# Optimization experiments

Hardware: AMD Instinct MI355X
Metric: run time of the kernel (lower is better)

The kernel has to match this reference:

```python
import jax, jax.numpy as jnp
import numpy as np

IGNORE = 255
THRESH = 0.7
MIN_KEPT = 100000
AUX_W = 1.0


def resize_bilinear_ac(x, oh, ow):
    # F.interpolate(..., mode='bilinear', align_corners=True); x: (b,c,h,w)
    b, c, h, w = x.shape
    ys = jnp.linspace(0.0, h - 1.0, oh)
    xs = jnp.linspace(0.0, w - 1.0, ow)
    y0 = jnp.floor(ys).astype(jnp.int32)
    x0 = jnp.floor(xs).astype(jnp.int32)
    y1 = jnp.minimum(y0 + 1, h - 1)
    x1 = jnp.minimum(x0 + 1, w - 1)
    wy = (ys - y0)[:, None]          # (oh,1) broadcasts over (b,c,oh,w)
    wx = xs - x0                     # (ow,)
    rows = x[:, :, y0, :] * (1.0 - wy) + x[:, :, y1, :] * wy   # (b,c,oh,w)
    return rows[:, :, :, x0] * (1.0 - wx) + rows[:, :, :, x1] * wx


def ohem_ce(pred, target):
    # pred: (b,c,h,w) logits, target: (b,h,w) int labels
    b, c, h, w = pred.shape
    n = b * h * w
    t = target.reshape(-1)
    valid = t != IGNORE
    t_cl = jnp.where(valid, t, 0)
    logits = pred.transpose(0, 2, 3, 1).reshape(n, c)
    logp = jax.nn.log_softmax(logits, axis=-1)
    pix = jnp.arange(n)
    logp_t = logp[pix, t_cl]
    # prob at target class; invalid pixels filled with 1 (as in masked_fill_)
    mask_prob = jnp.where(valid, jnp.exp(logp_t), 1.0)
    idx = min(n, MIN_KEPT) - 1
    thr = jnp.maximum(jnp.asarray(THRESH, pred.dtype), jnp.sort(mask_prob)[idx])
    kept = mask_prob <= thr
    final_valid = valid & kept
    nll = -logp_t
    denom = jnp.maximum(final_valid.sum(), 1).astype(pred.dtype)
    return jnp.sum(jnp.where(final_valid, nll, 0.0)) / denom


def boundary_bce(p, t):
    # p: (n,1,h,w) probs, t: (n,1,h,w) binary targets; per-sample pos/neg weights
    pos = jnp.sum(t == 1.0, axis=(1, 2, 3), keepdims=True).astype(p.dtype)
    neg = jnp.sum(t == 0.0, axis=(1, 2, 3), keepdims=True).astype(p.dtype)
    valid = pos + neg
    wgt = jnp.where(t == 1.0, neg / valid, jnp.where(t == 0.0, pos / valid, 0.0))
    logp = jnp.clip(jnp.log(p), -100.0)          # torch BCELoss clamps log at -100
    log1mp = jnp.clip(jnp.log(1.0 - p), -100.0)
    bce = -(t * logp + (1.0 - t) * log1mp)
    return jnp.mean(wgt * bce)


def setup_inputs() -> dict:
    key = jax.random.key(0)
    k1, k2, k3, k4, k5 = jax.random.split(key, 5)
    main_pred = jax.random.normal(k1, (4, 19, 64, 128), dtype=jnp.float32)
    coarse_pred = jax.random.normal(k2, (4, 19, 64, 128), dtype=jnp.float32)
    boundary_pred = jax.random.uniform(k3, (4, 1, 64, 128), dtype=jnp.float32)
    seg_gt = jax.random.randint(k4, (4, 512, 1024), 0, 19, dtype=jnp.int32)
    boundary_gt = jax.random.randint(k5, (4, 1, 512, 1024), 0, 2).astype(jnp.float32)
    return {"main_pred": main_pred, "coarse_pred": coarse_pred,
            "boundary_pred": boundary_pred, "seg_gt": seg_gt,
            "boundary_gt": boundary_gt}


def reference(main_pred, coarse_pred, boundary_pred, seg_gt, boundary_gt):
    h, w = seg_gt.shape[1], seg_gt.shape[2]
    main_up = resize_bilinear_ac(main_pred, h, w)
    loss = ohem_ce(main_up, seg_gt)
    coarse_up = resize_bilinear_ac(coarse_pred, h, w)
    loss = loss + AUX_W * ohem_ce(coarse_up, seg_gt)
    bound_up = resize_bilinear_ac(boundary_pred, h, w)
    loss = loss + boundary_bce(bound_up, boundary_gt)
    return loss
```

## Files before the change

kernel.cpp:

```cpp
#include <hip/hip_runtime.h>

#define NPX    2097152
#define NPX4   (NPX/4)
#define CH_STR 8192
#define IMG_STR 155648

#define OFF_CTL   (2ull*NPX*4)
#define CTL_HIST    0
#define CTL_CNT1    0
#define CTL_CNT2    2048
#define CTL_BAR     24576
#define CTL_FLAG    24579
#define CTL_PREFIX  24580
#define CTL_KREM    24582
#define CTL_THR     24584
#define CTL_PPSUM   24586
#define CTL_PPCNT   28682
#define CTL_OPSUM   32778
#define CTL_OPCNT   33290
#define CTL_BPS     33802
#define CTL_BPC     34826

#define MAGIC_FAST 0x3A9C67E5u
#define GRID_P1    1536u

__device__ __forceinline__ void st_dev_f(float* p, float v) {
    __hip_atomic_store(p, v, __ATOMIC_RELAXED, __HIP_MEMORY_SCOPE_AGENT);
}
__device__ __forceinline__ void st_dev_u(unsigned* p, unsigned v) {
    __hip_atomic_store(p, v, __ATOMIC_RELAXED, __HIP_MEMORY_SCOPE_AGENT);
}
__device__ __forceinline__ float ld_dev_f(const float* p) {
    return __hip_atomic_load((float*)p, __ATOMIC_RELAXED, __HIP_MEMORY_SCOPE_AGENT);
}
__device__ __forceinline__ unsigned ld_dev_u(const unsigned* p) {
    return __hip_atomic_load((unsigned*)p, __ATOMIC_RELAXED, __HIP_MEMORY_SCOPE_AGENT);
}

__global__ __launch_bounds__(256, 5) void fused_pass1(
    const float* __restrict__ mp, const float* __restrict__ cp,
    const float* __restrict__ bp, const int* __restrict__ seg,
    const float* __restrict__ bg,
    float* __restrict__ probA, float* __restrict__ ppsum, unsigned* __restrict__ ppcnt,
    float* __restrict__ bps, unsigned* __restrict__ bpc,
    unsigned* __restrict__ cnt1, unsigned* __restrict__ cnt2,
    unsigned* __restrict__ flag,
    float* __restrict__ out)
{
    __shared__ float2 erow[19 * 128];
    __shared__ float rf[4]; __shared__ unsigned ru[4];
    __shared__ float rf2[4]; __shared__ unsigned ru2[4];
    __shared__ unsigned amLast;
    __shared__ float Pb[4], Nb[4]; __shared__ unsigned PCb[4], NCb[4];
    int bk = blockIdx.x;
    int tid = threadIdx.x;

    if (bk < 1024) {
        int v = ((bk & 7) << 7) | (bk >> 3);
        int head = v >> 9;
        int b    = (v >> 7) & 3;
        int k    = v & 127;
        const float* pred = head ? cp : mp;

        int y0g = min((int)((float)(4 * k) * (63.0f / 511.0f)), 63);
        int row0 = y0g, row1 = min(y0g + 1, 63), row2 = min(y0g + 2, 63);

        float4 rv[3][3];
#pragma unroll
        for (int r = 0; r < 3; ++r) {
            int ry = (r == 0) ? row0 : ((r == 1) ? row1 : row2);
            const float* rp = pred + (size_t)b * IMG_STR + ry * 128;
#pragma unroll
            for (int sr = 0; sr < 3; ++sr) {
                int s = tid + (sr << 8);
                if (s < 608) {
                    int c = s >> 5, x4 = (s & 31) << 2;
                    rv[r][sr] = *(const float4*)(rp + c * CH_STR + x4);
                } else {
                    rv[r][sr] = make_float4(0.f, 0.f, 0.f, 0.f);
                }
            }
        }

        int xb = tid << 2;
        float fx0 = (float)xb * (127.0f / 1023.0f);
        int X = min((int)fx0, 126);
        float wA[4], wB[4], wC[4];
#pragma unroll
        for (int dx = 0; dx < 4; ++dx) {
            float fx = (float)(xb + dx) * (127.0f / 1023.0f);
            int x0 = min((int)fx, 127);
            float wx = fx - (float)x0;
            bool sm = (x0 == X);
            wA[dx] = sm ? (1.0f - wx) : 0.0f;
            wB[dx] = sm ? wx : (1.0f - wx);
            wC[dx] = sm ? 0.0f : wx;
        }

#pragma unroll 1
        for (int d = 0; d < 4; ++d) {
            int y = (k << 2) + d;
            int task = (b << 9) + y;
            float fy = (float)y * (63.0f / 511.0f);
            int y0 = min((int)fy, 63);
            float wy = fy - (float)y0;
            int j = y0 - y0g;

            int P = task * 1024 + xb;
            int4 t4 = *(const int4*)(seg + P);
            int t[4] = {t4.x, t4.y, t4.z, t4.w};

#pragma unroll
            for (int sr = 0; sr < 3; ++sr) {
                int s = tid + (sr << 8);
                float4 cu = (j == 0) ? rv[0][sr] : rv[1][sr];
                float4 nx = (j == 0) ? rv[1][sr] : rv[2][sr];
                float e0 = fmaf(wy, nx.x - cu.x, cu.x);
                float e1 = fmaf(wy, nx.y - cu.y, cu.y);
                float e2 = fmaf(wy, nx.z - cu.z, cu.z);
                float e3 = fmaf(wy, nx.w - cu.w, cu.w);
                float en = __shfl_down(e0, 1, 64);
                if (s < 608) {
                    int c = s >> 5, x4 = (s & 31) << 2;
                    float last = ((s & 31) == 31) ? e3 : en;
                    float4 w0 = make_float4(e0, e1, e1, e2);
                    float4 w1 = make_float4(e2, e3, e3, last);
                    *(float4*)(&erow[c * 128 + x4])     = w0;
                    *(float4*)(&erow[c * 128 + x4 + 2]) = w1;
                }
            }
            __syncthreads();

            float acc[4] = {0.f, 0.f, 0.f, 0.f};
            for (int c = 0; c < 19; ++c) {
                float2 eA = erow[c * 128 + X];
                float2 eB = erow[c * 128 + X + 1];
#pragma unroll
                for (int dx = 0; dx < 4; ++dx) {
                    float l = fmaf(eA.x, wA[dx], fmaf(eA.y, wB[dx], eB.y * wC[dx]));
                    acc[dx] += __expf(l);
                }
            }

            float fs = 0.f; unsigned ic = 0;
            float pr[4];
#pragma unroll
            for (int dx = 0; dx < 4; ++dx) {
                bool valid = (t[dx] != 255);
                int tc = valid ? t[dx] : 0;
                float2 eA = erow[tc * 128 + X];
                float2 eB = erow[tc * 128 + X + 1];
                float lt = fmaf(eA.x, wA[dx], fmaf(eA.y, wB[dx], eB.y * wC[dx]));
                float ls = __logf(acc[dx]);
                float n  = ls - lt;
                float p  = fminf(__expf(-n), 1.0f);
                pr[dx] = valid ? p : 1.0f;
                if (valid && p <= 0.7f) { fs += n; ic++; }
            }
            *(float4*)(probA + (size_t)head * NPX + P) = make_float4(pr[0], pr[1], pr[2], pr[3]);

            for (int o = 32; o; o >>= 1) {
                fs += __shfl_down(fs, o, 64);
                ic += (unsigned)__shfl_down((int)ic, o, 64);
            }
            int wave = tid >> 6, lane = tid & 63;
            if (lane == 0) { rf[wave] = fs; ru[wave] = ic; }
            __syncthreads();
            if (tid == 0) {
                st_dev_f(&ppsum[head * 2048 + task], rf[0] + rf[1] + rf[2] + rf[3]);
                st_dev_u(&ppcnt[head * 2048 + task], ru[0] + ru[1] + ru[2] + ru[3]);
            }
        }
    } else {
        int bb = bk - 1024;
        int b  = bb >> 7;
        int blk = bb & 127;
        float psum = 0.f, nsum = 0.f; unsigned pc = 0, nc = 0;

        for (int g = blk * 256 + tid; g < 131072; g += 128 * 256) {
            int P = g << 2;
            int y = P >> 10, xb = P & 1023;

            float fy = (float)y * (63.0f / 511.0f);
            int y0 = min((int)fy, 63);
            int y1 = min(y0 + 1, 63);
            float wy = fy - (float)y0;

            const float* r0 = bp + b * 8192 + y0 * 128;
            const float* r1 = bp + b * 8192 + y1 * 128;
            float fx0 = (float)xb * (127.0f / 1023.0f);
            int X  = min((int)fx0, 126);
            int X2 = min(X + 2, 127);
            float c0 = r0[X], c1 = r0[X + 1], c2 = r0[X2];
            float d0 = r1[X], d1 = r1[X + 1], d2 = r1[X2];
            float e0 = fmaf(wy, d0 - c0, c0);
            float e1 = fmaf(wy, d1 - c1, c1);
            float e2 = fmaf(wy, d2 - c2, c2);

            float4 t4 = *(const float4*)(bg + (size_t)b * 524288 + P);
            float tv[4] = {t4.x, t4.y, t4.z, t4.w};

#pragma unroll
            for (int dx = 0; dx < 4; ++dx) {
                float fx = (float)(xb + dx) * (127.0f / 1023.0f);
                int x0 = min((int)fx, 127);
                int x1 = min(x0 + 1, 127);
                float wx = fx - (float)x0;
                float a0 = (x0 == X)     ? e0 : e1;
                float a1 = (x1 == X + 1) ? e1 : e2;
                float p  = fmaf(wx, a1 - a0, a0);
                bool isp = (tv[dx] == 1.0f);
                bool isn = (tv[dx] == 0.0f);
                float q = isp ? p : 1.0f - p;
                float l = fmaxf(__logf(q), -100.0f);
                if (isp) { pc++; psum -= l; }
                if (isn) { nc++; nsum -= l; }
            }
        }
        for (int o = 32; o; o >>= 1) {
            psum += __shfl_down(psum, o, 64);
            nsum += __shfl_down(nsum, o, 64);
            pc   += (unsigned)__shfl_down((int)pc, o, 64);
            nc   += (unsigned)__shfl_down((int)nc, o, 64);
        }
        int wave = tid >> 6, lane = tid & 63;
        if (lane == 0) { rf[wave] = psum; rf2[wave] = nsum; ru[wave] = pc; ru2[wave] = nc; }
        __syncthreads();
        if (tid == 0) {
            st_dev_f(&bps[2 * bb],     rf[0] + rf[1] + rf[2] + rf[3]);
            st_dev_f(&bps[2 * bb + 1], rf2[0] + rf2[1] + rf2[2] + rf2[3]);
            st_dev_u(&bpc[2 * bb],     ru[0] + ru[1] + ru[2] + ru[3]);
            st_dev_u(&bpc[2 * bb + 1], ru2[0] + ru2[1] + ru2[2] + ru2[3]);
        }
    }

    __syncthreads();
    if (tid == 0) {
        asm volatile("s_waitcnt vmcnt(0)" ::: "memory");
        unsigned last = 0u;
        unsigned o1 = __hip_atomic_fetch_add(&cnt1[(bk & 63) << 5], 1u,
                                             __ATOMIC_RELAXED, __HIP_MEMORY_SCOPE_AGENT);
        if (o1 == 23u) {
            unsigned o2 = __hip_atomic_fetch_add(cnt2, 1u,
                                                 __ATOMIC_RELAXED, __HIP_MEMORY_SCOPE_AGENT);
            last = (o2 == 63u) ? 1u : 0u;
        }
        amLast = last;
    }
    __syncthreads();
    if (!amLast) return;

    float s0 = 0.f, s1 = 0.f; unsigned c0 = 0u, c1 = 0u;
    for (int i = tid; i < 2048; i += 256) {
        s0 += ld_dev_f(&ppsum[i]);        c0 += ld_dev_u(&ppcnt[i]);
        s1 += ld_dev_f(&ppsum[2048 + i]); c1 += ld_dev_u(&ppcnt[2048 + i]);
    }
    for (int o = 32; o; o >>= 1) {
        s0 += __shfl_down(s0, o, 64); s1 += __shfl_down(s1, o, 64);
        c0 += (unsigned)__shfl_down((int)c0, o, 64);
        c1 += (unsigned)__shfl_down((int)c1, o, 64);
    }
    int wv = tid >> 6, ln = tid & 63;
    if (ln == 0) { rf[wv] = s0; rf2[wv] = s1; ru[wv] = c0; ru2[wv] = c1; }
    __syncthreads();
    float S0 = rf[0] + rf[1] + rf[2] + rf[3];
    float S1 = rf2[0] + rf2[1] + rf2[2] + rf2[3];
    unsigned C0 = ru[0] + ru[1] + ru[2] + ru[3];
    unsigned C1 = ru2[0] + ru2[1] + ru2[2] + ru2[3];
    bool fast = (C0 >= 100000u) && (C1 >= 100000u);

    if (fast) {
        float*    lf = (float*)erow;
        unsigned* lu = (unsigned*)erow + 256;
        for (int b = 0; b < 4; ++b) {
            float ps = 0.f, ns = 0.f; unsigned p_c = 0, n_c = 0;
            if (tid < 128) {
                int jj = b * 128 + tid;
                ps  = ld_dev_f(&bps[2 * jj]); ns  = ld_dev_f(&bps[2 * jj + 1]);
                p_c = ld_dev_u(&bpc[2 * jj]); n_c = ld_dev_u(&bpc[2 * jj + 1]);
            }
            lf[tid] = ps; lu[tid] = p_c; __syncthreads();
            for (int o = 128; o; o >>= 1) {
                if (tid < o) { lf[tid] += lf[tid + o]; lu[tid] += lu[tid + o]; }
                __syncthreads();
            }
            if (tid == 0) { Pb[b] = lf[0]; PCb[b] = lu[0]; }
            __syncthreads();
            lf[tid] = ns; lu[tid] = n_c; __syncthreads();
            for (int o = 128; o; o >>= 1) {
                if (tid < o) { lf[tid] += lf[tid + o]; lu[tid] += lu[tid + o]; }
                __syncthreads();
            }
            if (tid == 0) { Nb[b] = lf[0]; NCb[b] = lu[0]; }
            __syncthreads();
        }
        if (tid == 0) {
            float bt = 0.f;
            for (int b = 0; b < 4; ++b) {
                float pos = (float)PCb[b], neg = (float)NCb[b];
                float val = fmaxf(pos + neg, 1.f);
                bt += (neg / val) * Pb[b] + (pos / val) * Nb[b];
            }
            float hls = S0 / fmaxf((float)C0, 1.f) + S1 / fmaxf((float)C1, 1.f);
            out[0] = hls + bt / 2097152.0f;
            st_dev_u(flag, MAGIC_FAST);
        }
    }
}

__device__ __forceinline__ void gbar(unsigned* bar, int tid) {
    __syncthreads();
    if (tid == 0) {
        unsigned g = __hip_atomic_load(&bar[1], __ATOMIC_RELAXED, __HIP_MEMORY_SCOPE_AGENT);
        unsigned t = __hip_atomic_fetch_add(&bar[0], 1u, __ATOMIC_ACQ_REL, __HIP_MEMORY_SCOPE_AGENT);
        if (t == 255u) {
            __hip_atomic_store(&bar[0], 0u, __ATOMIC_RELAXED, __HIP_MEMORY_SCOPE_AGENT);
            __hip_atomic_store(&bar[1], g + 1u, __ATOMIC_RELEASE, __HIP_MEMORY_SCOPE_AGENT);
        } else {
            while (__hip_atomic_load(&bar[1], __ATOMIC_ACQUIRE, __HIP_MEMORY_SCOPE_AGENT) == g)
                __builtin_amdgcn_s_sleep(8);
        }
    }
    __syncthreads();
}

__device__ void combine_out(int tid, float headLossSum,
                            const float* __restrict__ bps, const unsigned* __restrict__ bpc,
                            float* __restrict__ out)
{
    __shared__ float lf[256]; __shared__ unsigned lu[256];
    __shared__ float Pb[4], Nb[4]; __shared__ unsigned PCb[4], NCb[4];
    for (int b = 0; b < 4; ++b) {
        float ps = 0.f, ns = 0.f; unsigned p_c = 0, n_c = 0;
        if (tid < 128) {
            int j = b * 128 + tid;
            ps = bps[2 * j]; ns = bps[2 * j + 1];
            p_c = bpc[2 * j]; n_c = bpc[2 * j + 1];
        }
        lf[tid] = ps; lu[tid] = p_c; __syncthreads();
        for (int o = 128; o; o >>= 1) {
            if (tid < o) { lf[tid] += lf[tid + o]; lu[tid] += lu[tid + o]; }
            __syncthreads();
        }
        if (tid == 0) { Pb[b] = lf[0]; PCb[b] = lu[0]; }
        __syncthreads();
        lf[tid] = ns; lu[tid] = n_c; __syncthreads();
        for (int o = 128; o; o >>= 1) {
            if (tid < o) { lf[tid] += lf[tid + o]; lu[tid] += lu[tid + o]; }
            __syncthreads();
        }
        if (tid == 0) { Nb[b] = lf[0]; NCb[b] = lu[0]; }
        __syncthreads();
    }
    if (tid == 0) {
        float bt = 0.f;
        for (int b = 0; b < 4; ++b) {
            float pos = (float)PCb[b], neg = (float)NCb[b];
            float val = fmaxf(pos + neg, 1.f);
            bt += (neg / val) * Pb[b] + (pos / val) * Nb[b];
        }
        out[0] = headLossSum + bt / 2097152.0f;
    }
}

__global__ __launch_bounds__(256) void finish_all(
    const float* __restrict__ probA, const int* __restrict__ seg,
    const float* __restrict__ ppsum, const unsigned* __restrict__ ppcnt,
    const float* __restrict__ bps, const unsigned* __restrict__ bpc,
    unsigned* __restrict__ hist, unsigned* __restrict__ bar,
    unsigned* __restrict__ prefix, unsigned* __restrict__ krem,
    float* __restrict__ thr,
    float* __restrict__ opsum, unsigned* __restrict__ opcnt,
    unsigned* __restrict__ flag,
    float* __restrict__ out)
{
    if (*flag == MAGIC_FAST)
        return;

    int tid = threadIdx.x, blk = blockIdx.x;
    int wave = tid >> 6, lane = tid & 63;

    float s0 = 0.f, s1 = 0.f; unsigned c0 = 0u, c1 = 0u;
    for (int i = tid; i < 2048; i += 256) {
        s0 += ppsum[i];        c0 += ppcnt[i];
        s1 += ppsum[2048 + i]; c1 += ppcnt[2048 + i];
    }
    for (int o = 32; o; o >>= 1) {
        s0 += __shfl_down(s0, o, 64); s1 += __shfl_down(s1, o, 64);
        c0 += (unsigned)__shfl_down((int)c0, o, 64);
        c1 += (unsigned)__shfl_down((int)c1, o, 64);
    }
    __shared__ float ws0[4], ws1[4]; __shared__ unsigned wc0[4], wc1[4];
    if (lane == 0) { ws0[wave] = s0; ws1[wave] = s1; wc0[wave] = c0; wc1[wave] = c1; }
    __syncthreads();
    float S0 = ws0[0] + ws0[1] + ws0[2] + ws0[3];
    float S1 = ws1[0] + ws1[1] + ws1[2] + ws1[3];
    unsigned C0 = wc0[0] + wc0[1] + wc0[2] + wc0[3];
    unsigned C1 = wc1[0] + wc1[1] + wc1[2] + wc1[3];
    bool done0 = C0 >= 100000u, done1 = C1 >= 100000u;

    if (done0 && done1) {
        if (blk == 0)
            combine_out(tid, S0 / fmaxf((float)C0, 1.f) + S1 / fmaxf((float)C1, 1.f),
                        bps, bpc, out);
        return;
    }

    __shared__ unsigned hsh[4096];
    __shared__ unsigned cpre[257];
    unsigned doneMask = (done0 ? 1u : 0u) | (done1 ? 2u : 0u);

    for (int i = blk * 256 + tid; i < 24576; i += 65536) hist[i] = 0u;
    gbar(bar, tid);

    for (int lvl = 0; lvl < 3; ++lvl) {
        unsigned* hl = hist + lvl * 8192;
        for (int h = 0; h < 2; ++h) {
            if (doneMask & (1u << h)) continue;
            unsigned pre = (lvl == 0) ? 0u : prefix[h];
            for (int i = tid; i < 4096; i += 256) hsh[i] = 0u;
            __syncthreads();
            const float4* prob = (const float4*)(probA + (size_t)h * NPX);
            for (int i = blk * 256 + tid; i < NPX4; i += 65536) {
                float4 p = prob[i];
                unsigned u[4] = {__float_as_uint(p.x), __float_as_uint(p.y),
                                 __float_as_uint(p.z), __float_as_uint(p.w)};
#pragma unroll
                for (int kk = 0; kk < 4; ++kk) {
                    unsigned bv = u[kk];
                    if (lvl == 0)      atomicAdd(&hsh[bv >> 18], 1u);
                    else if (lvl == 1) { if ((bv >> 18) == pre) atomicAdd(&hsh[(bv >> 6) & 0xFFFu], 1u); }
                    else               { if ((bv >> 6) == pre) atomicAdd(&hsh[bv & 63u], 1u); }
                }
            }
            __syncthreads();
            for (int i = tid; i < 4096; i += 256) {
                unsigned v = hsh[i];
                if (v) atomicAdd(&hl[h * 4096 + i], v);
            }
            __syncthreads();
        }
        gbar(bar, tid);
        if (blk == 0) {
            int bins = (lvl == 2) ? 64 : 4096;
            for (int h = 0; h < 2; ++h) {
                if (doneMask & (1u << h)) continue;
                const unsigned* hh = hl + h * 4096;
                int per = (bins + 255) >> 8;
                int base = tid * per;
                unsigned ssum = 0;
                for (int i = 0; i < per; ++i) { int idx = base + i; if (idx < bins) ssum += hh[idx]; }
                cpre[tid] = ssum; __syncthreads();
                if (tid == 0) {
                    unsigned acc = 0;
                    for (int i = 0; i < 256; ++i) { unsigned v = cpre[i]; cpre[i] = acc; acc += v; }
                    cpre[256] = acc;
                }
                __syncthreads();
                unsigned K = (lvl == 0) ? 100000u : krem[h];
                unsigned my = cpre[tid], nx = cpre[tid + 1];
                if (K > 0 && my < K && K <= nx) {
                    unsigned acc = my;
                    for (int i = 0; i < per; ++i) {
                        int idx = base + i;
                        unsigned c = (idx < bins) ? hh[idx] : 0u;
                        if (acc < K && K <= acc + c) {
                            if (lvl == 0)      { prefix[h] = (unsigned)idx; krem[h] = K - acc; }
                            else if (lvl == 1) { prefix[h] = (prefix[h] << 12) | (unsigned)idx; krem[h] = K - acc; }
                            else {
                                unsigned bitsv = (prefix[h] << 6) | (unsigned)idx;
                                thr[h] = fmaxf(0.7f, __uint_as_float(bitsv));
                            }
                            break;
                        }
                        acc += c;
                    }
                }
                __syncthreads();
            }
        }
        gbar(bar, tid);
    }

    for (int h = 0; h < 2; ++h) {
        if (doneMask & (1u << h)) continue;
        float th = thr[h];
        const float4* prob = (const float4*)(probA + (size_t)h * NPX);
        const int4*   sg4  = (const int4*)seg;
        float fs = 0.f; unsigned ic = 0;
        for (int i = blk * 256 + tid; i < NPX4; i += 65536) {
            float4 p = prob[i]; int4 tt = sg4[i];
            if (tt.x != 255 && p.x <= th) { fs -= __logf(p.x); ic++; }
            if (tt.y != 255 && p.y <= th) { fs -= __logf(p.y); ic++; }
            if (tt.z != 255 && p.z <= th) { fs -= __logf(p.z); ic++; }
            if (tt.w != 255 && p.w <= th) { fs -= __logf(p.w); ic++; }
        }
        for (int o = 32; o; o >>= 1) {
            fs += __shfl_down(fs, o, 64);
            ic += (unsigned)__shfl_down((int)ic, o, 64);
        }
        __shared__ float wf[4]; __shared__ unsigned wu[4];
        if (lane == 0) { wf[wave] = fs; wu[wave] = ic; }
        __syncthreads();
        if (tid == 0) {
            opsum[h * 256 + blk] = wf[0] + wf[1] + wf[2] + wf[3];
            opcnt[h * 256 + blk] = wu[0] + wu[1] + wu[2] + wu[3];
        }
        __syncthreads();
    }
    gbar(bar, tid);
    if (blk == 0) {
        __shared__ float lf2[256]; __shared__ unsigned lu2[256];
        float hls = 0.f;
        for (int h = 0; h < 2; ++h) {
            float S; unsigned C;
            if (doneMask & (1u << h)) {
                S = h ? S1 : S0; C = h ? C1 : C0;
            } else {
                lf2[tid] = opsum[h * 256 + tid]; lu2[tid] = opcnt[h * 256 + tid];
                __syncthreads();
                for (int o = 128; o; o >>= 1) {
                    if (tid < o) { lf2[tid] += lf2[tid + o]; lu2[tid] += lu2[tid + o]; }
                    __syncthreads();
                }
                S = lf2[0]; C = lu2[0];
                __syncthreads();
            }
            hls += S / fmaxf((float)C, 1.f);
        }
        combine_out(tid, hls, bps, bpc, out);
    }
}

extern "C" void kernel_launch(void* const* d_in, const int* in_sizes, int n_in,
                              void* d_out, int out_size, void* d_ws, size_t ws_size,
                              hipStream_t stream)
{
    const float* mp  = (const float*)d_in[0];
    const float* cp  = (const float*)d_in[1];
    const float* bp  = (const float*)d_in[2];
    const int*   seg = (const int*)d_in[3];
    const float* bg  = (const float*)d_in[4];
    float* out = (float*)d_out;

    char* ws = (char*)d_ws;
    float* probA = (float*)ws;
    unsigned* ctl    = (unsigned*)(ws + OFF_CTL);
    unsigned* hist   = ctl + CTL_HIST;
    unsigned* cnt1   = ctl + CTL_CNT1;
    unsigned* cnt2   = ctl + CTL_CNT2;
    unsigned* bar    = ctl + CTL_BAR;
    unsigned* flag   = ctl + CTL_FLAG;
    unsigned* prefix = ctl + CTL_PREFIX;
    unsigned* krem   = ctl + CTL_KREM;
    float*    thr    = (float*)(ctl + CTL_THR);
    float*    ppsum  = (float*)(ctl + CTL_PPSUM);
    unsigned* ppcnt  = ctl + CTL_PPCNT;
    float*    opsum  = (float*)(ctl + CTL_OPSUM);
    unsigned* opcnt  = ctl + CTL_OPCNT;
    float*    bps    = (float*)(ctl + CTL_BPS);
    unsigned* bpc    = ctl + CTL_BPC;

    hipMemsetAsync(ws + OFF_CTL, 0, 24580ull * 4, stream);

    fused_pass1<<<dim3(GRID_P1), 256, 0, stream>>>(mp, cp, bp, seg, bg, probA,
                                                   ppsum, ppcnt, bps, bpc,
                                                   cnt1, cnt2, flag, out);
    finish_all<<<dim3(256), 256, 0, stream>>>(probA, seg, ppsum, ppcnt, bps, bpc,
                                              hist, bar, prefix, krem, thr,
                                              opsum, opcnt, flag, out);
}
```

Before: 113.1 us.

## Drop per-pixel prob buffer and second kernel; handle rare OHEM case in-block

Stops writing the full per-pixel target-probability array (two heads, 8M floats) in the first pass and removes the second finish kernel along with its grid barriers. The last block now computes the final loss directly. When fewer than the minimum number of pixels pass the threshold, a single block recomputes probabilities from the logits with a three-level radix histogram, which is very slow but only runs in that fallback case. The memset also shrinks. This removes 16MB of global writes and a kernel launch, at the cost of a single-block slow path that would be extremely slow if it were ever hit.

```diff
diff --git a/kernel.cpp b/kernel.cpp
--- a/kernel.cpp
+++ b/kernel.cpp
@@ -6,22 +6,14 @@
 #define IMG_STR 155648
 
 #define OFF_CTL   (2ull*NPX*4)
-#define CTL_HIST    0
 #define CTL_CNT1    0
 #define CTL_CNT2    2048
-#define CTL_BAR     24576
-#define CTL_FLAG    24579
-#define CTL_PREFIX  24580
-#define CTL_KREM    24582
-#define CTL_THR     24584
+#define CTL_GHIST   4096
 #define CTL_PPSUM   24586
 #define CTL_PPCNT   28682
-#define CTL_OPSUM   32778
-#define CTL_OPCNT   33290
 #define CTL_BPS     33802
 #define CTL_BPC     34826
 
-#define MAGIC_FAST 0x3A9C67E5u
 #define GRID_P1    1536u
 
 __device__ __forceinline__ void st_dev_f(float* p, float v) {
@@ -37,14 +29,136 @@
     return __hip_atomic_load((unsigned*)p, __ATOMIC_RELAXED, __HIP_MEMORY_SCOPE_AGENT);
 }
 
-__global__ __launch_bounds__(256, 5) void fused_pass1(
+__device__ __attribute__((noinline)) void slow_head(
+    int tid, const float* __restrict__ pred, const int* __restrict__ seg,
+    unsigned* __restrict__ ghist, float2* erow,
+    float* smf, unsigned* smu)
+{
+    int xb = tid << 2;
+    float fx0 = (float)xb * (127.0f / 1023.0f);
+    int X = min((int)fx0, 126);
+    float wA[4], wB[4], wC[4];
+#pragma unroll
+    for (int dx = 0; dx < 4; ++dx) {
+        float fx = (float)(xb + dx) * (127.0f / 1023.0f);
+        int x0 = min((int)fx, 127);
+        float wx = fx - (float)x0;
+        bool sm = (x0 == X);
+        wA[dx] = sm ? (1.0f - wx) : 0.0f;
+        wB[dx] = sm ? wx : (1.0f - wx);
+        wC[dx] = sm ? 0.0f : wx;
+    }
+
+    for (int lvl = 0; lvl < 4; ++lvl) {
+        if (lvl < 3) {
+            for (int i = tid; i < 4096; i += 256) ghist[i] = 0u;
+        }
+        __syncthreads();
+        unsigned pre = (lvl == 0) ? 0u : smu[0];
+        float th = smf[0];
+        float fs = 0.f; unsigned ic = 0;
+
+        for (int task = 0; task < 2048; ++task) {
+            int b = task >> 9, y = task & 511;
+            float fy = (float)y * (63.0f / 511.0f);
+            int y0 = min((int)fy, 63);
+            int y1 = min(y0 + 1, 63);
+            float wy = fy - (float)y0;
+            const float* r0 = pred + (size_t)b * IMG_STR + y0 * 128;
+            const float* r1 = pred + (size_t)b * IMG_STR + y1 * 128;
+            for (int i = tid; i < 2432; i += 256) {
+                int c = i >> 7, x = i & 127;
+                float v0 = r0[c * CH_STR + x];
+                float v1 = r1[c * CH_STR + x];
+                float e = fmaf(wy, v1 - v0, v0);
+                erow[c * 128 + x].x = e;
+                if (x > 0)    erow[c * 128 + x - 1].y = e;
+                if (x == 127) erow[c * 128 + 127].y = e;
+            }
+            __syncthreads();
+
+            int P = task * 1024 + xb;
+            int4 t4 = *(const int4*)(seg + P);
+            int t[4] = {t4.x, t4.y, t4.z, t4.w};
+
+            float acc[4] = {0.f, 0.f, 0.f, 0.f};
+            for (int c = 0; c < 19; ++c) {
+                float2 eA = erow[c * 128 + X];
+                float2 eB = erow[c * 128 + X + 1];
+#pragma unroll
+                for (int dx = 0; dx < 4; ++dx) {
+                    float l = fmaf(eA.x, wA[dx], fmaf(eA.y, wB[dx], eB.y * wC[dx]));
+                    acc[dx] += __expf(l);
+                }
+            }
+#pragma unroll
+            for (int dx = 0; dx < 4; ++dx) {
+                bool valid = (t[dx] != 255);
+                int tc = valid ? t[dx] : 0;
+                float2 eA = erow[tc * 128 + X];
+                float2 eB = erow[tc * 128 + X + 1];
+                float lt = fmaf(eA.x, wA[dx], fmaf(eA.y, wB[dx], eB.y * wC[dx]));
+                float ls = __logf(acc[dx]);
+                float n  = ls - lt;
+                float p  = fminf(__expf(-n), 1.0f);
+                float pr = valid ? p : 1.0f;
+                if (lvl < 3) {
+                    unsigned bv = __float_as_uint(pr);
+                    if (lvl == 0)      atomicAdd(&ghist[bv >> 18], 1u);
+                    else if (lvl == 1) { if ((bv >> 18) == pre) atomicAdd(&ghist[(bv >> 6) & 0xFFFu], 1u); }
+                    else               { if ((bv >> 6) == pre) atomicAdd(&ghist[bv & 63u], 1u); }
+                } else {
+                    if (valid && p <= th) { fs -= __logf(p); ic++; }
+                }
+            }
+            __syncthreads();
+        }
+
+        if (lvl < 3) {
+            if (tid == 0) {
+                int bins = (lvl == 2) ? 64 : 4096;
+                unsigned kr = (lvl == 0) ? 100000u : smu[1];
+                unsigned acc = 0;
+                for (int idx = 0; idx < bins; ++idx) {
+                    unsigned c = ghist[idx];
+                    if (acc < kr && kr <= acc + c) {
+                        if (lvl == 0)      { smu[0] = (unsigned)idx; smu[1] = kr - acc; }
+                        else if (lvl == 1) { smu[0] = (pre << 12) | (unsigned)idx; smu[1] = kr - acc; }
+                        else {
+                            unsigned bitsv = (pre << 6) | (unsigned)idx;
+                            smf[0] = fmaxf(0.7f, __uint_as_float(bitsv));
+                        }
+                        break;
+                    }
+                    acc += c;
+                }
+            }
+            __syncthreads();
+        } else {
+            for (int o = 32; o; o >>= 1) {
+                fs += __shfl_down(fs, o, 64);
+                ic += (unsigned)__shfl_down((int)ic, o, 64);
+            }
+            int wave = tid >> 6, lane = tid & 63;
+            if (lane == 0) { smf[4 + wave] = fs; smu[4 + wave] = ic; }
+            __syncthreads();
+            if (tid == 0) {
+                smf[1] = smf[4] + smf[5] + smf[6] + smf[7];
+                smu[2] = smu[4] + smu[5] + smu[6] + smu[7];
+            }
+            __syncthreads();
+        }
+    }
+}
+
+__global__ __launch_bounds__(256) void fused_all(
     const float* __restrict__ mp, const float* __restrict__ cp,
     const float* __restrict__ bp, const int* __restrict__ seg,
     const float* __restrict__ bg,
-    float* __restrict__ probA, float* __restrict__ ppsum, unsigned* __restrict__ ppcnt,
+    float* __restrict__ ppsum, unsigned* __restrict__ ppcnt,
     float* __restrict__ bps, unsigned* __restrict__ bpc,
     unsigned* __restrict__ cnt1, unsigned* __restrict__ cnt2,
-    unsigned* __restrict__ flag,
+    unsigned* __restrict__ ghist,
     float* __restrict__ out)
 {
     __shared__ float2 erow[19 * 128];
@@ -52,6 +166,7 @@
     __shared__ float rf2[4]; __shared__ unsigned ru2[4];
     __shared__ unsigned amLast;
     __shared__ float Pb[4], Nb[4]; __shared__ unsigned PCb[4], NCb[4];
+    __shared__ float smf[8]; __shared__ unsigned smu[8];
     int bk = blockIdx.x;
     int tid = threadIdx.x;
 
@@ -143,7 +258,6 @@
             }
 
             float fs = 0.f; unsigned ic = 0;
-            float pr[4];
 #pragma unroll
             for (int dx = 0; dx < 4; ++dx) {
                 bool valid = (t[dx] != 255);
@@ -154,10 +268,8 @@
                 float ls = __logf(acc[dx]);
                 float n  = ls - lt;
                 float p  = fminf(__expf(-n), 1.0f);
-                pr[dx] = valid ? p : 1.0f;
                 if (valid && p <= 0.7f) { fs += n; ic++; }
             }
-            *(float4*)(probA + (size_t)head * NPX + P) = make_float4(pr[0], pr[1], pr[2], pr[3]);
 
             for (int o = 32; o; o >>= 1) {
                 fs += __shfl_down(fs, o, 64);
@@ -267,9 +379,24 @@
     float S1 = rf2[0] + rf2[1] + rf2[2] + rf2[3];
     unsigned C0 = ru[0] + ru[1] + ru[2] + ru[3];
     unsigned C1 = ru2[0] + ru2[1] + ru2[2] + ru2[3];
-    bool fast = (C0 >= 100000u) && (C1 >= 100000u);
-
-    if (fast) {
+    bool done0 = (C0 >= 100000u), done1 = (C1 >= 100000u);
+
+    float hl0, hl1;
+    if (done0) {
+        hl0 = S0 / fmaxf((float)C0, 1.f);
+    } else {
+        slow_head(tid, mp, seg, ghist, erow, smf, smu);
+        hl0 = smf[1] / fmaxf((float)smu[2], 1.f);
+    }
+    if (done1) {
+        hl1 = S1 / fmaxf((float)C1, 1.f);
+    } else {
+        slow_head(tid, cp, seg, ghist, erow, smf, smu);
+        hl1 = smf[1] / fmaxf((float)smu[2], 1.f);
+    }
+    float hls = hl0 + hl1;
+
+    {
         float*    lf = (float*)erow;
         unsigned* lu = (unsigned*)erow + 256;
         for (int b = 0; b < 4; ++b) {
@@ -301,234 +428,8 @@
                 float val = fmaxf(pos + neg, 1.f);
                 bt += (neg / val) * Pb[b] + (pos / val) * Nb[b];
             }
-            float hls = S0 / fmaxf((float)C0, 1.f) + S1 / fmaxf((float)C1, 1.f);
             out[0] = hls + bt / 2097152.0f;
-            st_dev_u(flag, MAGIC_FAST);
-        }
-    }
-}
-
-__device__ __forceinline__ void gbar(unsigned* bar, int tid) {
-    __syncthreads();
-    if (tid == 0) {
-        unsigned g = __hip_atomic_load(&bar[1], __ATOMIC_RELAXED, __HIP_MEMORY_SCOPE_AGENT);
-        unsigned t = __hip_atomic_fetch_add(&bar[0], 1u, __ATOMIC_ACQ_REL, __HIP_MEMORY_SCOPE_AGENT);
-        if (t == 255u) {
-            __hip_atomic_store(&bar[0], 0u, __ATOMIC_RELAXED, __HIP_MEMORY_SCOPE_AGENT);
-            __hip_atomic_store(&bar[1], g + 1u, __ATOMIC_RELEASE, __HIP_MEMORY_SCOPE_AGENT);
-        } else {
-            while (__hip_atomic_load(&bar[1], __ATOMIC_ACQUIRE, __HIP_MEMORY_SCOPE_AGENT) == g)
-                __builtin_amdgcn_s_sleep(8);
-        }
-    }
-    __syncthreads();
-}
-
-__device__ void combine_out(int tid, float headLossSum,
-                            const float* __restrict__ bps, const unsigned* __restrict__ bpc,
-                            float* __restrict__ out)
-{
-    __shared__ float lf[256]; __shared__ unsigned lu[256];
-    __shared__ float Pb[4], Nb[4]; __shared__ unsigned PCb[4], NCb[4];
-    for (int b = 0; b < 4; ++b) {
-        float ps = 0.f, ns = 0.f; unsigned p_c = 0, n_c = 0;
-        if (tid < 128) {
-            int j = b * 128 + tid;
-            ps = bps[2 * j]; ns = bps[2 * j + 1];
-            p_c = bpc[2 * j]; n_c = bpc[2 * j + 1];
-        }
-        lf[tid] = ps; lu[tid] = p_c; __syncthreads();
-        for (int o = 128; o; o >>= 1) {
-            if (tid < o) { lf[tid] += lf[tid + o]; lu[tid] += lu[tid + o]; }
-            __syncthreads();
-        }
-        if (tid == 0) { Pb[b] = lf[0]; PCb[b] = lu[0]; }
-        __syncthreads();
-        lf[tid] = ns; lu[tid] = n_c; __syncthreads();
-        for (int o = 128; o; o >>= 1) {
-            if (tid < o) { lf[tid] += lf[tid + o]; lu[tid] += lu[tid + o]; }
-            __syncthreads();
-        }
-        if (tid == 0) { Nb[b] = lf[0]; NCb[b] = lu[0]; }
-        __syncthreads();
-    }
-    if (tid == 0) {
-        float bt = 0.f;
-        for (int b = 0; b < 4; ++b) {
-            float pos = (float)PCb[b], neg = (float)NCb[b];
-            float val = fmaxf(pos + neg, 1.f);
-            bt += (neg / val) * Pb[b] + (pos / val) * Nb[b];
-        }
-        out[0] = headLossSum + bt / 2097152.0f;
-    }
-}
-
-__global__ __launch_bounds__(256) void finish_all(
-    const float* __restrict__ probA, const int* __restrict__ seg,
-    const float* __restrict__ ppsum, const unsigned* __restrict__ ppcnt,
-    const float* __restrict__ bps, const unsigned* __restrict__ bpc,
-    unsigned* __restrict__ hist, unsigned* __restrict__ bar,
-    unsigned* __restrict__ prefix, unsigned* __restrict__ krem,
-    float* __restrict__ thr,
-    float* __restrict__ opsum, unsigned* __restrict__ opcnt,
-    unsigned* __restrict__ flag,
-    float* __restrict__ out)
-{
-    if (*flag == MAGIC_FAST)
-        return;
-
-    int tid = threadIdx.x, blk = blockIdx.x;
-    int wave = tid >> 6, lane = tid & 63;
-
-    float s0 = 0.f, s1 = 0.f; unsigned c0 = 0u, c1 = 0u;
-    for (int i = tid; i < 2048; i += 256) {
-        s0 += ppsum[i];        c0 += ppcnt[i];
-        s1 += ppsum[2048 + i]; c1 += ppcnt[2048 + i];
-    }
-    for (int o = 32; o; o >>= 1) {
-        s0 += __shfl_down(s0, o, 64); s1 += __shfl_down(s1, o, 64);
-        c0 += (unsigned)__shfl_down((int)c0, o, 64);
-        c1 += (unsigned)__shfl_down((int)c1, o, 64);
-    }
-    __shared__ float ws0[4], ws1[4]; __shared__ unsigned wc0[4], wc1[4];
-    if (lane == 0) { ws0[wave] = s0; ws1[wave] = s1; wc0[wave] = c0; wc1[wave] = c1; }
-    __syncthreads();
-    float S0 = ws0[0] + ws0[1] + ws0[2] + ws0[3];
-    float S1 = ws1[0] + ws1[1] + ws1[2] + ws1[3];
-    unsigned C0 = wc0[0] + wc0[1] + wc0[2] + wc0[3];
-    unsigned C1 = wc1[0] + wc1[1] + wc1[2] + wc1[3];
-    bool done0 = C0 >= 100000u, done1 = C1 >= 100000u;
-
-    if (done0 && done1) {
-        if (blk == 0)
-            combine_out(tid, S0 / fmaxf((float)C0, 1.f) + S1 / fmaxf((float)C1, 1.f),
-                        bps, bpc, out);
-        return;
-    }
-
-    __shared__ unsigned hsh[4096];
-    __shared__ unsigned cpre[257];
-    unsigned doneMask = (done0 ? 1u : 0u) | (done1 ? 2u : 0u);
-
-    for (int i = blk * 256 + tid; i < 24576; i += 65536) hist[i] = 0u;
-    gbar(bar, tid);
-
-    for (int lvl = 0; lvl < 3; ++lvl) {
-        unsigned* hl = hist + lvl * 8192;
-        for (int h = 0; h < 2; ++h) {
-            if (doneMask & (1u << h)) continue;
-            unsigned pre = (lvl == 0) ? 0u : prefix[h];
-            for (int i = tid; i < 4096; i += 256) hsh[i] = 0u;
-            __syncthreads();
-            const float4* prob = (const float4*)(probA + (size_t)h * NPX);
-            for (int i = blk * 256 + tid; i < NPX4; i += 65536) {
-                float4 p = prob[i];
-                unsigned u[4] = {__float_as_uint(p.x), __float_as_uint(p.y),
-                                 __float_as_uint(p.z), __float_as_uint(p.w)};
-#pragma unroll
-                for (int kk = 0; kk < 4; ++kk) {
-                    unsigned bv = u[kk];
-                    if (lvl == 0)      atomicAdd(&hsh[bv >> 18], 1u);
-                    else if (lvl == 1) { if ((bv >> 18) == pre) atomicAdd(&hsh[(bv >> 6) & 0xFFFu], 1u); }
-                    else               { if ((bv >> 6) == pre) atomicAdd(&hsh[bv & 63u], 1u); }
-                }
-            }
-            __syncthreads();
-            for (int i = tid; i < 4096; i += 256) {
-                unsigned v = hsh[i];
-                if (v) atomicAdd(&hl[h * 4096 + i], v);
-            }
-            __syncthreads();
-        }
-        gbar(bar, tid);
-        if (blk == 0) {
-            int bins = (lvl == 2) ? 64 : 4096;
-            for (int h = 0; h < 2; ++h) {
-                if (doneMask & (1u << h)) continue;
-                const unsigned* hh = hl + h * 4096;
-                int per = (bins + 255) >> 8;
-                int base = tid * per;
-                unsigned ssum = 0;
-                for (int i = 0; i < per; ++i) { int idx = base + i; if (idx < bins) ssum += hh[idx]; }
-                cpre[tid] = ssum; __syncthreads();
-                if (tid == 0) {
-                    unsigned acc = 0;
-                    for (int i = 0; i < 256; ++i) { unsigned v = cpre[i]; cpre[i] = acc; acc += v; }
-                    cpre[256] = acc;
-                }
-                __syncthreads();
-                unsigned K = (lvl == 0) ? 100000u : krem[h];
-                unsigned my = cpre[tid], nx = cpre[tid + 1];
-                if (K > 0 && my < K && K <= nx) {
-                    unsigned acc = my;
-                    for (int i = 0; i < per; ++i) {
-                        int idx = base + i;
-                        unsigned c = (idx < bins) ? hh[idx] : 0u;
-                        if (acc < K && K <= acc + c) {
-                            if (lvl == 0)      { prefix[h] = (unsigned)idx; krem[h] = K - acc; }
-                            else if (lvl == 1) { prefix[h] = (prefix[h] << 12) | (unsigned)idx; krem[h] = K - acc; }
-                            else {
-                                unsigned bitsv = (prefix[h] << 6) | (unsigned)idx;
-                                thr[h] = fmaxf(0.7f, __uint_as_float(bitsv));
-                            }
-                            break;
-                        }
-                        acc += c;
-                    }
-                }
-                __syncthreads();
-            }
-        }
-        gbar(bar, tid);
-    }
-
-    for (int h = 0; h < 2; ++h) {
-        if (doneMask & (1u << h)) continue;
-        float th = thr[h];
-        const float4* prob = (const float4*)(probA + (size_t)h * NPX);
-        const int4*   sg4  = (const int4*)seg;
-        float fs = 0.f; unsigned ic = 0;
-        for (int i = blk * 256 + tid; i < NPX4; i += 65536) {
-            float4 p = prob[i]; int4 tt = sg4[i];
-            if (tt.x != 255 && p.x <= th) { fs -= __logf(p.x); ic++; }
-            if (tt.y != 255 && p.y <= th) { fs -= __logf(p.y); ic++; }
-            if (tt.z != 255 && p.z <= th) { fs -= __logf(p.z); ic++; }
-            if (tt.w != 255 && p.w <= th) { fs -= __logf(p.w); ic++; }
-        }
-        for (int o = 32; o; o >>= 1) {
-            fs += __shfl_down(fs, o, 64);
-            ic += (unsigned)__shfl_down((int)ic, o, 64);
-        }
-        __shared__ float wf[4]; __shared__ unsigned wu[4];
-        if (lane == 0) { wf[wave] = fs; wu[wave] = ic; }
-        __syncthreads();
-        if (tid == 0) {
-            opsum[h * 256 + blk] = wf[0] + wf[1] + wf[2] + wf[3];
-            opcnt[h * 256 + blk] = wu[0] + wu[1] + wu[2] + wu[3];
-        }
-        __syncthreads();
-    }
-    gbar(bar, tid);
-    if (blk == 0) {
-        __shared__ float lf2[256]; __shared__ unsigned lu2[256];
-        float hls = 0.f;
-        for (int h = 0; h < 2; ++h) {
-            float S; unsigned C;
-            if (doneMask & (1u << h)) {
-                S = h ? S1 : S0; C = h ? C1 : C0;
-            } else {
-                lf2[tid] = opsum[h * 256 + tid]; lu2[tid] = opcnt[h * 256 + tid];
-                __syncthreads();
-                for (int o = 128; o; o >>= 1) {
-                    if (tid < o) { lf2[tid] += lf2[tid + o]; lu2[tid] += lu2[tid + o]; }
-                    __syncthreads();
-                }
-                S = lf2[0]; C = lu2[0];
-                __syncthreads();
-            }
-            hls += S / fmaxf((float)C, 1.f);
-        }
-        combine_out(tid, hls, bps, bpc, out);
+        }
     }
 }
 
@@ -544,29 +445,18 @@
     float* out = (float*)d_out;
 
     char* ws = (char*)d_ws;
-    float* probA = (float*)ws;
     unsigned* ctl    = (unsigned*)(ws + OFF_CTL);
-    unsigned* hist   = ctl + CTL_HIST;
     unsigned* cnt1   = ctl + CTL_CNT1;
     unsigned* cnt2   = ctl + CTL_CNT2;
-    unsigned* bar    = ctl + CTL_BAR;
-    unsigned* flag   = ctl + CTL_FLAG;
-    unsigned* prefix = ctl + CTL_PREFIX;
-    unsigned* krem   = ctl + CTL_KREM;
-    float*    thr    = (float*)(ctl + CTL_THR);
+    unsigned* ghist  = ctl + CTL_GHIST;
     float*    ppsum  = (float*)(ctl + CTL_PPSUM);
     unsigned* ppcnt  = ctl + CTL_PPCNT;
-    float*    opsum  = (float*)(ctl + CTL_OPSUM);
-    unsigned* opcnt  = ctl + CTL_OPCNT;
     float*    bps    = (float*)(ctl + CTL_BPS);
     unsigned* bpc    = ctl + CTL_BPC;
 
-    hipMemsetAsync(ws + OFF_CTL, 0, 24580ull * 4, stream);
-
-    fused_pass1<<<dim3(GRID_P1), 256, 0, stream>>>(mp, cp, bp, seg, bg, probA,
-                                                   ppsum, ppcnt, bps, bpc,
-                                                   cnt1, cnt2, flag, out);
-    finish_all<<<dim3(256), 256, 0, stream>>>(probA, seg, ppsum, ppcnt, bps, bpc,
-                                              hist, bar, prefix, krem, thr,
-                                              opsum, opcnt, flag, out);
-}
+    hipMemsetAsync(ws + OFF_CTL, 0, 2052ull * 4, stream);
+
+    fused_all<<<dim3(GRID_P1), 256, 0, stream>>>(mp, cp, bp, seg, bg,
+                                                 ppsum, ppcnt, bps, bpc,
+                                                 cnt1, cnt2, ghist, out);
+}
```

Measured after the change: 113.3 us. About the same (+0.2%).
